# Performance work log

Measured on AMD Instinct MI355X. Metric: run time of the kernel, lower is better.

The kernel has to match this reference:

```python
import jax, jax.numpy as jnp
import numpy as np

OUTPUT_SIZE = 65
THRESHOLD = 0.2
EPS = 1e-6


def setup_inputs() -> dict:
    key = jax.random.key(0)
    x = jax.random.normal(key, (64, 4, 512), dtype=jnp.float32)
    return {"x": x}


def _valid_mask(x):
    # True from first nonzero to last nonzero along L, per (n, c); all False if row is all-zero.
    N, C, L = x.shape
    nz = x != 0
    any_nz = nz.any(axis=2, keepdims=True)            # [N, C, 1]
    first = jnp.argmax(nz, axis=2)                    # [N, C]
    last = (L - 1) - jnp.argmax(nz[:, :, ::-1], axis=2)
    idx = jnp.arange(L)
    mask = (idx[None, None, :] >= first[:, :, None]) & (idx[None, None, :] <= last[:, :, None])
    return mask & any_nz                              # [N, C, L] bool


def reference(x):
    N, C, L = x.shape
    mask = _valid_mask(x)
    mf = mask.astype(x.dtype)
    cnt = jnp.clip(mf.sum(axis=2), 1, None)           # [N, C]
    mean = (x * mf).sum(axis=2) / cnt                 # [N, C]
    var = (((x * mf - mean[..., None]) ** 2) * mf).sum(axis=2) / cnt
    std = jnp.sqrt(var)                               # [N, C]
    x_norm = (x - mean[..., None]) / jnp.clip(std, EPS, None)[..., None]
    x_norm = jnp.where(mask, x_norm, jnp.zeros((), x.dtype))  # [N, C, L]
    # Recurrence plot: cdist on 1-d points == |x_i - x_j|, thresholded.
    dist = jnp.abs(x_norm[..., :, None] - x_norm[..., None, :])  # [N, C, L, L]
    rp = (dist < THRESHOLD).astype(x.dtype)
    size = min(L, OUTPUT_SIZE)
    out = jnp.zeros((N, C, OUTPUT_SIZE, OUTPUT_SIZE), dtype=x.dtype)
    out = out.at[:, :, :size, :size].set(rp[:, :, :size, :size])
    return out
```

## Files before the change

### kernel.cpp

```cpp
#include <hip/hip_runtime.h>
#include <climits>

#define LROW 512
#define OUT_S 65
#define NOUT (OUT_S * OUT_S)
#define THRESH 0.2f
#define EPS_F 1e-6f

typedef float f4 __attribute__((ext_vector_type(4)));

__global__ __launch_bounds__(256) void rp_kernel(const float* __restrict__ x,
                                                 float* __restrict__ out) {
    const int row  = blockIdx.x;
    const int tid  = threadIdx.x;
    const int lane = tid & 63;
    const int wid  = tid >> 6;
    const float* xr = x + (size_t)row * LROW;
    const f4* xr4   = reinterpret_cast<const f4*>(xr);

    const f4 a = xr4[lane];
    const f4 b = xr4[lane + 64];

    int lo = INT_MAX, hi = -1;
    double s1 = 0.0, s2 = 0.0;
    #pragma unroll
    for (int e = 0; e < 4; ++e) {
        const int   k0 = 4 * lane + e;
        const float va = a[e];
        if (va != 0.0f) { lo = min(lo, k0); hi = max(hi, k0); }
        s1 += (double)va; s2 += (double)va * (double)va;
        const int   k1 = k0 + 256;
        const float vb = b[e];
        if (vb != 0.0f) { lo = min(lo, k1); hi = max(hi, k1); }
        s1 += (double)vb; s2 += (double)vb * (double)vb;
    }

    #pragma unroll
    for (int off = 32; off > 0; off >>= 1) {
        lo = min(lo, __shfl_xor(lo, off, 64));
        hi = max(hi, __shfl_xor(hi, off, 64));
        s1 += __shfl_xor(s1, off, 64);
        s2 += __shfl_xor(s2, off, 64);
    }

    const bool   anyNZ = (hi >= 0);
    const double cnt   = anyNZ ? (double)(hi - lo + 1) : 1.0;
    const float  mean  = (float)(s1 / cnt);
    const double dm    = (double)mean;
    double var = (s2 - 2.0 * dm * s1 + cnt * dm * dm) / cnt;
    var = var > 0.0 ? var : 0.0;
    const float stdc = fmaxf(sqrtf((float)var), EPS_F);

    __shared__ float xnw[4][68];
    if (lane < 17) {
        f4 w;
        #pragma unroll
        for (int e = 0; e < 4; ++e) {
            const int  k = 4 * lane + e;
            const bool m = anyNZ && (k >= lo) && (k <= hi);
            w[e] = m ? (a[e] - mean) / stdc : 0.0f;
        }
        *reinterpret_cast<f4*>(&xnw[wid][4 * lane]) = w;
    }
    asm volatile("s_waitcnt lgkmcnt(0)" ::: "memory");

    const float* xn = xnw[wid];
    float* orow = out + (size_t)row * NOUT;

    const int h      = (4 - (row & 3)) & 3;
    const int nbody  = (NOUT - h) >> 2;
    const int t0     = h + (nbody << 2);
    const int ntail  = NOUT - t0;

    if (tid < h) {
        orow[tid] = (fabsf(xn[0] - xn[tid]) < THRESH) ? 1.0f : 0.0f;
    }
    if (tid >= 4 && tid - 4 < ntail) {
        const int k = t0 + (tid - 4);
        const int i = k / OUT_S;
        const int j = k - i * OUT_S;
        orow[k] = (fabsf(xn[i] - xn[j]) < THRESH) ? 1.0f : 0.0f;
    }

    for (int g = tid; g < nbody; g += 256) {
        const int e0 = h + 4 * g;
        const int i  = e0 / OUT_S;
        int   jj  = e0 - i * OUT_S;
        float xii = xn[i];
        f4 r;
        #pragma unroll
        for (int e = 0; e < 4; ++e) {
            if (jj == OUT_S) { jj = 0; xii = xn[i + 1]; }
            r[e] = (fabsf(xii - xn[jj]) < THRESH) ? 1.0f : 0.0f;
            ++jj;
        }
        *reinterpret_cast<f4*>(orow + e0) = r;
    }
}

extern "C" void kernel_launch(void* const* d_in, const int* in_sizes, int n_in,
                              void* d_out, int out_size, void* d_ws, size_t ws_size,
                              hipStream_t stream) {
    const float* x  = (const float*)d_in[0];
    float*      out = (float*)d_out;
    const int rows  = in_sizes[0] / LROW;
    rp_kernel<<<rows, 256, 0, stream>>>(x, out);
}
```

Baseline: 10.99 us.

## Split each row's output across four blocks by output-row ranges

Launches four blocks per (n,c) row, each writing a contiguous range of roughly 16 output rows of the 65x65 recurrence plot, with per-range alignment head and tail handling. Every block still loads the full input row and recomputes the bounds and statistics redundantly. The aim is more blocks (1024 instead of 256) to fill the GPU's CUs and spread the store traffic, at the price of four times the input reads and reduction work.

```diff
diff --git a/kernel.cpp b/kernel.cpp
--- a/kernel.cpp
+++ b/kernel.cpp
@@ -11,7 +11,9 @@
 
 __global__ __launch_bounds__(256) void rp_kernel(const float* __restrict__ x,
                                                  float* __restrict__ out) {
-    const int row  = blockIdx.x;
+    const int bid  = blockIdx.x;
+    const int row  = bid >> 2;
+    const int q    = bid & 3;
     const int tid  = threadIdx.x;
     const int lane = tid & 63;
     const int wid  = tid >> 6;
@@ -67,25 +69,36 @@
     const float* xn = xnw[wid];
     float* orow = out + (size_t)row * NOUT;
 
-    const int h      = (4 - (row & 3)) & 3;
-    const int nbody  = (NOUT - h) >> 2;
-    const int t0     = h + (nbody << 2);
-    const int ntail  = NOUT - t0;
+    const int rstart = (q == 0) ? 0 : (16 * q + 1);
+    const int rend   = rstart + ((q == 0) ? 17 : 16);
+    const int e0 = rstart * OUT_S;
+    const int e1 = rend * OUT_S;
+
+    const int mis = (int)(((size_t)row * NOUT + (size_t)e0) & 3);
+    int h = (4 - mis) & 3;
+    if (h > e1 - e0) h = e1 - e0;
+    const int bstart = e0 + h;
+    const int nbody  = (e1 - bstart) >> 2;
+    const int t0     = bstart + (nbody << 2);
+    const int ntail  = e1 - t0;
 
     if (tid < h) {
-        orow[tid] = (fabsf(xn[0] - xn[tid]) < THRESH) ? 1.0f : 0.0f;
+        const int k = e0 + tid;
+        const int i = k / OUT_S;
+        const int j = k - i * OUT_S;
+        orow[k] = (fabsf(xn[i] - xn[j]) < THRESH) ? 1.0f : 0.0f;
     }
-    if (tid >= 4 && tid - 4 < ntail) {
-        const int k = t0 + (tid - 4);
+    if (tid >= 8 && tid - 8 < ntail) {
+        const int k = t0 + (tid - 8);
         const int i = k / OUT_S;
         const int j = k - i * OUT_S;
         orow[k] = (fabsf(xn[i] - xn[j]) < THRESH) ? 1.0f : 0.0f;
     }
 
     for (int g = tid; g < nbody; g += 256) {
-        const int e0 = h + 4 * g;
-        const int i  = e0 / OUT_S;
-        int   jj  = e0 - i * OUT_S;
+        const int es = bstart + 4 * g;
+        const int i  = es / OUT_S;
+        int   jj  = es - i * OUT_S;
         float xii = xn[i];
         f4 r;
         #pragma unroll
@@ -94,7 +107,7 @@
             r[e] = (fabsf(xii - xn[jj]) < THRESH) ? 1.0f : 0.0f;
             ++jj;
         }
-        *reinterpret_cast<f4*>(orow + e0) = r;
+        *reinterpret_cast<f4*>(orow + es) = r;
     }
 }
 
@@ -104,5 +117,5 @@
     const float* x  = (const float*)d_in[0];
     float*      out = (float*)d_out;
     const int rows  = in_sizes[0] / LROW;
-    rp_kernel<<<rows, 256, 0, stream>>>(x, out);
+    rp_kernel<<<rows * 4, 256, 0, stream>>>(x, out);
 }
```

Result: slower. 11.50 us (+4.7%).
